# Kernel tuning notes

Hardware: AMD Instinct MI355X
Metric: run time of the kernel (lower is better)

Reference implementation:

```python
import jax, jax.numpy as jnp
import numpy as np

N_NODES = 50000
N_EDGES = 800000
D_IN, HIDDEN, OUT, K = 96, 64, 16, 3


def _glorot(key, shape):
    fan_in, fan_out = shape[-2], shape[-1]
    lim = (6.0 / (fan_in + fan_out)) ** 0.5
    return jax.random.uniform(key, shape, jnp.float32, -lim, lim)


def setup_inputs() -> dict:
    key = jax.random.key(0)
    k1, k2, k3, k4 = jax.random.split(key, 4)
    x = jax.random.normal(k1, (N_NODES, D_IN), dtype=jnp.float32)
    edge_index = jax.random.randint(k2, (2, N_EDGES), 0, N_NODES, dtype=jnp.int64)
    # ChebConv params: K stacked linear maps per layer + one bias per layer
    W1 = _glorot(k3, (K, D_IN, HIDDEN))
    b1 = jnp.zeros((HIDDEN,), jnp.float32)
    W2 = _glorot(k4, (K, HIDDEN, OUT))
    b2 = jnp.zeros((OUT,), jnp.float32)
    return {"x": x, "edge_index": edge_index, "W1": W1, "b1": b1, "W2": W2, "b2": b2}


def _cheb_norm(edge_index, num_nodes):
    # PyG ChebConv norm with normalization='sym', lambda_max=2.0:
    # Ltilde = (2/lmax)*(I - D^-1/2 A D^-1/2) - I = -D^-1/2 A D^-1/2 (diag weight 0)
    src, dst = edge_index[0], edge_index[1]
    ones = jnp.ones((edge_index.shape[1],), jnp.float32)
    deg = jax.ops.segment_sum(ones, src, num_segments=num_nodes)
    dis = jnp.where(deg > 0, jax.lax.rsqrt(jnp.maximum(deg, 1.0)), 0.0)
    return -dis[src] * dis[dst]  # [E]


def _cheb_conv(x, src, dst, w, W, b, num_nodes):
    # Chebyshev recurrence: Tx0=x, Tx1=L x, Txk=2 L Tx_{k-1} - Tx_{k-2}
    def prop(h):  # sparse matvec: scatter-add of weighted source features
        return jax.ops.segment_sum(w[:, None] * h[src], dst, num_segments=num_nodes)

    Tx0 = x
    out = Tx0 @ W[0]
    Tx1 = prop(Tx0)
    out = out + Tx1 @ W[1]
    for k in range(2, W.shape[0]):
        Tx2 = 2.0 * prop(Tx1) - Tx0
        out = out + Tx2 @ W[k]
        Tx0, Tx1 = Tx1, Tx2
    return out + b


def reference(x, edge_index, W1, b1, W2, b2):
    num_nodes = x.shape[0]
    src, dst = edge_index[0], edge_index[1]
    w = _cheb_norm(edge_index, num_nodes)
    h = jax.nn.relu(_cheb_conv(x, src, dst, w, W1, b1, num_nodes))
    return _cheb_conv(h, src, dst, w, W2, b2, num_nodes)
```

## Files before the change

kernel.cpp:

```cpp
#include <hip/hip_runtime.h>

#define N_NODES 50000
#define N_EDGES 800000
#define D_IN 96
#define HID 64
#define D_OUT 16

#define EPB 2048
#define NBLK_E ((N_EDGES + EPB - 1) / EPB)
#define BSHIFT 7
#define NBKT ((N_NODES + 127) / 128)
#define DCAP 2560
#define PACK_TOT (3 * D_IN * HID + 3 * HID * D_OUT)
#define PACK_BLKS (PACK_TOT / 256)

typedef unsigned short u16;
typedef unsigned int u32;
typedef __attribute__((ext_vector_type(4))) float f32x4;
typedef __attribute__((ext_vector_type(8))) short bf16x8;

__device__ inline float bflo(u32 v) { union { u32 i; float f; } u; u.i = v << 16; return u.f; }
__device__ inline float bfhi(u32 v) { union { u32 i; float f; } u; u.i = v & 0xffff0000u; return u.f; }
__device__ inline u16 f2bf(float f) {
    union { float f; u32 i; } u; u.f = f;
    return (u16)((u.i + 0x7fffu + ((u.i >> 16) & 1u)) >> 16);
}
__device__ inline u32 pack2(float lo, float hi) {
    return (u32)f2bf(lo) | ((u32)f2bf(hi) << 16);
}


__global__ __launch_bounds__(256)
void passA(const int* __restrict__ src, const int* __restrict__ dst,
           int* __restrict__ blk_cnt_src, int* __restrict__ blk_cnt_dst,
           const float* __restrict__ W1, const float* __restrict__ W2,
           u16* __restrict__ Pb1, u16* __restrict__ Pb2) {
    const int t = threadIdx.x, blk = blockIdx.x;
    if (blk >= NBLK_E) {
        int tt = (blk - NBLK_E) * 256 + t;
        if (tt < 3 * D_IN * HID) {
            int j = tt & 7, rest = tt >> 3;
            int c = rest % 192, i = (rest / 192) * 8 + j;
            int kc = c / 64, o = c % 64;
            Pb1[tt] = f2bf(W1[((long)kc * D_IN + i) * HID + o]);
        } else if (tt < PACK_TOT) {
            int t2 = tt - 3 * D_IN * HID;
            int j = t2 & 7, rest = t2 >> 3;
            int c = rest % 48, i = (rest / 48) * 8 + j;
            int kc = c / 16, o = c % 16;
            Pb2[t2] = f2bf(W2[((long)kc * HID + i) * D_OUT + o]);
        }
        return;
    }
    __shared__ int hs[NBKT], hd[NBKT];
    for (int i = t; i < NBKT; i += 256) { hs[i] = 0; hd[i] = 0; }
    __syncthreads();
    const int e0 = blk * EPB;
    const int e1 = (e0 + EPB < N_EDGES) ? e0 + EPB : N_EDGES;
    for (int e = e0 + t; e < e1; e += 256) {
        atomicAdd(&hs[src[e] >> BSHIFT], 1);
        atomicAdd(&hd[dst[e] >> BSHIFT], 1);
    }
    __syncthreads();
    for (int b = t; b < NBKT; b += 256) {
        blk_cnt_src[b * NBLK_E + blk] = hs[b];
        blk_cnt_dst[b * NBLK_E + blk] = hd[b];
    }
}

__global__ __launch_bounds__(64)
void passB(int* __restrict__ blk_cnt_src, int* __restrict__ blk_cnt_dst,
           int* __restrict__ tot_src, int* __restrict__ tot_dst) {
    const int b = blockIdx.x;
    int* cnt; int* tot;
    if (b < NBKT) { cnt = blk_cnt_dst + b * NBLK_E;          tot = tot_dst + b; }
    else          { cnt = blk_cnt_src + (b - NBKT) * NBLK_E; tot = tot_src + (b - NBKT); }
    const int lane = threadIdx.x;
    int carry = 0;
    for (int base0 = 0; base0 < NBLK_E; base0 += 64) {
        int i = base0 + lane;
        int v = (i < NBLK_E) ? cnt[i] : 0;
        int incl = v;
        #pragma unroll
        for (int off = 1; off < 64; off <<= 1) {
            int x = __shfl_up(incl, off);
            if (lane >= off) incl += x;
        }
        if (i < NBLK_E) cnt[i] = carry + incl - v;
        carry += __shfl(incl, 63);
    }
    if (lane == 0) *tot = carry;
}

__global__ __launch_bounds__(256)
void passB2(const int* __restrict__ tot_src, const int* __restrict__ tot_dst,
            int* __restrict__ base_src, int* __restrict__ base_dst, int* __restrict__ row_ptr) {
    __shared__ int s[512];
    const int t = threadIdx.x;
    for (int pass = 0; pass < 2; ++pass) {
        const int* tot = pass ? tot_src : tot_dst;
        int* bas = pass ? base_src : base_dst;
        s[t]       = (t < NBKT) ? tot[t] : 0;
        s[t + 256] = (t + 256 < NBKT) ? tot[t + 256] : 0;
        __syncthreads();
        for (int off = 1; off < 512; off <<= 1) {
            int a1 = (t >= off) ? s[t - off] : 0;
            int a2 = (t + 256 >= off) ? s[t + 256 - off] : 0;
            __syncthreads();
            s[t] += a1; s[t + 256] += a2;
            __syncthreads();
        }
        if (t == 0) bas[0] = 0;
        if (t < NBKT) bas[t + 1] = s[t];
        if (t + 256 < NBKT) bas[t + 257] = s[t + 256];
        __syncthreads();
    }
    if (t == 0) row_ptr[N_NODES] = N_EDGES;
}

__global__ __launch_bounds__(256)
void passC(const int* __restrict__ src, const int* __restrict__ dst,
           const int* __restrict__ blk_off_src, const int* __restrict__ blk_off_dst,
           const int* __restrict__ base_src, const int* __restrict__ base_dst,
           u16* __restrict__ sorted_srconly, u32* __restrict__ sorted_pair) {
    __shared__ int cs[NBKT], cd[NBKT];
    const int t = threadIdx.x, blk = blockIdx.x;
    for (int b = t; b < NBKT; b += 256) {
        cs[b] = base_src[b] + blk_off_src[b * NBLK_E + blk];
        cd[b] = base_dst[b] + blk_off_dst[b * NBLK_E + blk];
    }
    __syncthreads();
    const int e0 = blk * EPB;
    const int e1 = (e0 + EPB < N_EDGES) ? e0 + EPB : N_EDGES;
    for (int e = e0 + t; e < e1; e += 256) {
        int sv = src[e], dv = dst[e];
        int ps = atomicAdd(&cs[sv >> BSHIFT], 1);
        sorted_srconly[ps] = (u16)sv;
        int pd = atomicAdd(&cd[dv >> BSHIFT], 1);
        sorted_pair[pd] = ((u32)dv << 16) | (u32)sv;
    }
}

__global__ __launch_bounds__(256)
void passD(const int* __restrict__ base_src, const u16* __restrict__ sorted_srconly,
           const int* __restrict__ base_dst, const u32* __restrict__ sorted_pair,
           float* __restrict__ dis, int* __restrict__ row_ptr, u16* __restrict__ wsrc) {
    const int t = threadIdx.x;
    if (blockIdx.x < NBKT) {
        __shared__ int hist[128];
        const int b = blockIdx.x;
        if (t < 128) hist[t] = 0;
        __syncthreads();
        const int eb = base_src[b], ee = base_src[b + 1];
        for (int i = eb + t; i < ee; i += 256)
            atomicAdd(&hist[sorted_srconly[i] & 127], 1);
        __syncthreads();
        const int node = (b << BSHIFT) + t;
        if (t < 128 && node < N_NODES) {
            int c = hist[t];
            dis[node] = c > 0 ? rsqrtf((float)c) : 0.0f;
        }
        return;
    }
    __shared__ u32 s_p[DCAP];
    __shared__ int hist[128];
    __shared__ int cur[128];
    const int b = blockIdx.x - NBKT;
    if (t < 128) hist[t] = 0;
    __syncthreads();
    const int eb = base_dst[b], ee = base_dst[b + 1];
    const int cnt = ee - eb;
    const int stage = cnt < DCAP ? cnt : DCAP;
    for (int i = t; i < stage; i += 256) {
        u32 v = sorted_pair[eb + i];
        s_p[i] = v;
        atomicAdd(&hist[(v >> 16) & 127], 1);
    }
    for (int i = stage + t; i < cnt; i += 256)
        atomicAdd(&hist[(sorted_pair[eb + i] >> 16) & 127], 1);
    __syncthreads();
    if (t < 64) {
        int v0 = hist[2 * t], v1 = hist[2 * t + 1];
        int p = v0 + v1;
        int incl = p;
        #pragma unroll
        for (int off = 1; off < 64; off <<= 1) {
            int x = __shfl_up(incl, off);
            if (t >= off) incl += x;
        }
        int excl = incl - p;
        cur[2 * t] = excl;
        cur[2 * t + 1] = excl + v0;
        int node = (b << BSHIFT) + 2 * t;
        if (node < N_NODES) row_ptr[node] = eb + excl;
        if (node + 1 < N_NODES) row_ptr[node + 1] = eb + excl + v0;
    }
    __syncthreads();
    for (int i = t; i < stage; i += 256) {
        u32 v = s_p[i];
        int slot = atomicAdd(&cur[(v >> 16) & 127], 1);
        wsrc[eb + slot] = (u16)(v & 0xFFFF);
    }
    for (int i = stage + t; i < cnt; i += 256) {
        u32 v = sorted_pair[eb + i];
        int slot = atomicAdd(&cur[(v >> 16) & 127], 1);
        wsrc[eb + slot] = (u16)(v & 0xFFFF);
    }
}


template<int K, int NC, int LDZ, int CPK, long CBS, bool AF32>
__global__ __launch_bounds__(256)
void gemm_mfma(const void* __restrict__ Av, const u16* __restrict__ P, u16* __restrict__ Z,
               const float* __restrict__ dis, u16* __restrict__ Zs) {
    constexpr int KT = K / 32;
    constexpr int TOT = K * NC;
    __shared__ u16 sP[TOT];
    for (int idx = threadIdx.x * 8; idx < TOT; idx += 2048)
        *(uint4*)&sP[idx] = *(const uint4*)&P[idx];
    __syncthreads();
    const int lane = threadIdx.x & 63;
    const int tile = blockIdx.x * 4 + (threadIdx.x >> 6);
    if (tile * 16 >= N_NODES) return;
    const int node0 = tile * 16;
    const int sub = lane >> 4, r16 = lane & 15;
    float dis4[4];
    #pragma unroll
    for (int r = 0; r < 4; ++r) dis4[r] = dis[node0 + sub * 4 + r];
    bf16x8 a[KT];
    if (AF32) {
        const float* ar = (const float*)Av + (long)(node0 + r16) * K + sub * 8;
        #pragma unroll
        for (int kt = 0; kt < KT; ++kt) {
            float4 a0 = *(const float4*)(ar + kt * 32);
            float4 a1 = *(const float4*)(ar + kt * 32 + 4);
            union { bf16x8 v; uint4 q; } u;
            u.q.x = pack2(a0.x, a0.y); u.q.y = pack2(a0.z, a0.w);
            u.q.z = pack2(a1.x, a1.y); u.q.w = pack2(a1.z, a1.w);
            a[kt] = u.v;
        }
    } else {
        const u16* ar = (const u16*)Av + (long)(node0 + r16) * K + sub * 8;
        #pragma unroll
        for (int kt = 0; kt < KT; ++kt)
            a[kt] = *(const bf16x8*)(ar + kt * 32);
    }
    #pragma unroll
    for (int ct = 0; ct < NC / 16; ++ct) {
        f32x4 acc = {0.f, 0.f, 0.f, 0.f};
        #pragma unroll
        for (int kt = 0; kt < KT; ++kt) {
            bf16x8 bfr = *(const bf16x8*)&sP[((kt * 4 + sub) * NC + ct * 16 + r16) * 8];
            acc = __builtin_amdgcn_mfma_f32_16x16x32_bf16(a[kt], bfr, acc, 0, 0, 0);
        }
        const long rowoff = (long)(node0 + sub * 4) * LDZ + (ct % CPK) * 16 + r16;
        u16* zp = Z + (long)(ct / CPK) * CBS + rowoff;
        #pragma unroll
        for (int r = 0; r < 4; ++r)
            zp[(long)r * LDZ] = f2bf(acc[r]);
        if (ct / CPK == 2) {
            u16* zs = Zs + rowoff;
            #pragma unroll
            for (int r = 0; r < 4; ++r)
                zs[(long)r * LDZ] = f2bf(acc[r] * dis4[r]);
        }
    }
}


#define EPI_S 0
#define EPI_H 1
#define EPI_OUT 2

__device__ inline void sum8(float (&acc)[8], uint4 q) {
    acc[0] += bflo(q.x); acc[1] += bfhi(q.x);
    acc[2] += bflo(q.y); acc[3] += bfhi(q.y);
    acc[4] += bflo(q.z); acc[5] += bfhi(q.z);
    acc[6] += bflo(q.w); acc[7] += bfhi(q.w);
}

template<int F, int NPB, int CAP, int EPI>
__global__ __launch_bounds__(256)
void gather_prop(const int* __restrict__ row_ptr, const u16* __restrict__ ws,
                 const u16* __restrict__ g,
                 const u16* __restrict__ aux1,
                 const u16* __restrict__ aux2,
                 const float* __restrict__ bias,
                 const float* __restrict__ dis,
                 void* __restrict__ outp) {
    __shared__ u16 s_p[CAP];
    __shared__ int s_beg[NPB + 1];
    const int tid = threadIdx.x;
    const int node0 = blockIdx.x * NPB;
    if (tid <= NPB) {
        int n = node0 + tid;
        s_beg[tid] = row_ptr[n > N_NODES ? N_NODES : n];
    }
    __syncthreads();
    const int ebeg = s_beg[0];
    const int cnt = s_beg[NPB] - ebeg;
    const int stage = cnt < CAP ? cnt : CAP;
    for (int e = tid; e < stage; e += 256)
        s_p[e] = ws[ebeg + e];
    __syncthreads();
    constexpr int CPN = F / 8;
    const int nl = tid / CPN;
    const int node = node0 + nl;
    if (nl >= NPB || node >= N_NODES) return;
    const int c8 = (tid % CPN) * 8;
    float acc[8];
    #pragma unroll
    for (int j = 0; j < 8; ++j) acc[j] = 0.0f;
    const int beg = s_beg[nl] - ebeg;
    const int end = s_beg[nl + 1] - ebeg;
    const int mid = end < stage ? end : stage;
    int e = beg;
    for (; e + 8 <= mid; e += 8) {
        int p0 = s_p[e],     p1 = s_p[e + 1], p2 = s_p[e + 2], p3 = s_p[e + 3];
        int p4 = s_p[e + 4], p5 = s_p[e + 5], p6 = s_p[e + 6], p7 = s_p[e + 7];
        uint4 q0 = *(const uint4*)(g + (long)p0 * F + c8);
        uint4 q1 = *(const uint4*)(g + (long)p1 * F + c8);
        uint4 q2 = *(const uint4*)(g + (long)p2 * F + c8);
        uint4 q3 = *(const uint4*)(g + (long)p3 * F + c8);
        uint4 q4 = *(const uint4*)(g + (long)p4 * F + c8);
        uint4 q5 = *(const uint4*)(g + (long)p5 * F + c8);
        uint4 q6 = *(const uint4*)(g + (long)p6 * F + c8);
        uint4 q7 = *(const uint4*)(g + (long)p7 * F + c8);
        sum8(acc, q0); sum8(acc, q1); sum8(acc, q2); sum8(acc, q3);
        sum8(acc, q4); sum8(acc, q5); sum8(acc, q6); sum8(acc, q7);
    }
    for (; e + 4 <= mid; e += 4) {
        int p0 = s_p[e], p1 = s_p[e + 1], p2 = s_p[e + 2], p3 = s_p[e + 3];
        uint4 q0 = *(const uint4*)(g + (long)p0 * F + c8);
        uint4 q1 = *(const uint4*)(g + (long)p1 * F + c8);
        uint4 q2 = *(const uint4*)(g + (long)p2 * F + c8);
        uint4 q3 = *(const uint4*)(g + (long)p3 * F + c8);
        sum8(acc, q0); sum8(acc, q1); sum8(acc, q2); sum8(acc, q3);
    }
    for (; e < mid; ++e)
        sum8(acc, *(const uint4*)(g + (long)s_p[e] * F + c8));
    for (e = (beg > stage ? beg : stage); e < end; ++e)
        sum8(acc, *(const uint4*)(g + (long)ws[ebeg + e] * F + c8));
    const float dd = dis[node];
    if (EPI == EPI_S) {
        const float m1 = dd, m2 = -2.0f * dd * dd;
        const uint4 z1 = *(const uint4*)(aux1 + (long)node * F + c8);
        uint4 r;
        r.x = pack2(fmaf(m1, bflo(z1.x), m2 * acc[0]), fmaf(m1, bfhi(z1.x), m2 * acc[1]));
        r.y = pack2(fmaf(m1, bflo(z1.y), m2 * acc[2]), fmaf(m1, bfhi(z1.y), m2 * acc[3]));
        r.z = pack2(fmaf(m1, bflo(z1.z), m2 * acc[4]), fmaf(m1, bfhi(z1.z), m2 * acc[5]));
        r.w = pack2(fmaf(m1, bflo(z1.w), m2 * acc[6]), fmaf(m1, bfhi(z1.w), m2 * acc[7]));
        *(uint4*)((u16*)outp + (long)node * F + c8) = r;
    } else {
        const uint4 z0 = *(const uint4*)(aux1 + (long)node * F + c8);
        const uint4 z2 = *(const uint4*)(aux2 + (long)node * F + c8);
        const float* bb = bias + c8;
        float v0 = bflo(z0.x) - bflo(z2.x) - dd * acc[0] + bb[0];
        float v1 = bfhi(z0.x) - bfhi(z2.x) - dd * acc[1] + bb[1];
        float v2 = bflo(z0.y) - bflo(z2.y) - dd * acc[2] + bb[2];
        float v3 = bfhi(z0.y) - bfhi(z2.y) - dd * acc[3] + bb[3];
        float v4 = bflo(z0.z) - bflo(z2.z) - dd * acc[4] + bb[4];
        float v5 = bfhi(z0.z) - bfhi(z2.z) - dd * acc[5] + bb[5];
        float v6 = bflo(z0.w) - bflo(z2.w) - dd * acc[6] + bb[6];
        float v7 = bfhi(z0.w) - bfhi(z2.w) - dd * acc[7] + bb[7];
        if (EPI == EPI_H) {
            uint4 r;
            r.x = pack2(fmaxf(v0, 0.f), fmaxf(v1, 0.f));
            r.y = pack2(fmaxf(v2, 0.f), fmaxf(v3, 0.f));
            r.z = pack2(fmaxf(v4, 0.f), fmaxf(v5, 0.f));
            r.w = pack2(fmaxf(v6, 0.f), fmaxf(v7, 0.f));
            *(uint4*)((u16*)outp + (long)node * F + c8) = r;
        } else {
            float* op = (float*)outp + (long)node * F + c8;
            *(float4*)op = make_float4(v0, v1, v2, v3);
            *(float4*)(op + 4) = make_float4(v4, v5, v6, v7);
        }
    }
}


extern "C" void kernel_launch(void* const* d_in, const int* in_sizes, int n_in,
                              void* d_out, int out_size, void* d_ws, size_t ws_size,
                              hipStream_t stream) {
    const float* x  = (const float*)d_in[0];
    const int*   ei = (const int*)d_in[1];
    const float* W1 = (const float*)d_in[2];
    const float* b1 = (const float*)d_in[3];
    const float* W2 = (const float*)d_in[4];
    const float* b2 = (const float*)d_in[5];
    const int* src = ei;
    const int* dst = ei + N_EDGES;

    float* dis          = (float*)d_ws;
    int*   row_ptr      = (int*)(dis + N_NODES);
    int*   blk_cnt_src  = row_ptr + 50016;
    int*   blk_cnt_dst  = blk_cnt_src + 152896;
    int*   tot_src      = blk_cnt_dst + 152896;
    int*   tot_dst      = tot_src + 512;
    int*   base_src     = tot_dst + 512;
    int*   base_dst     = base_src + 512;
    u16*   srconly      = (u16*)(base_dst + 512);
    u32*   sorted_pair  = (u32*)(srconly + N_EDGES);
    u16*   wsrc         = (u16*)(sorted_pair + N_EDGES);
    u16*   Z            = wsrc + N_EDGES;
    u16*   Zs           = Z  + (long)3 * N_NODES * HID;
    u16*   S            = Zs + (long)N_NODES * HID;
    u16*   hb           = S  + (long)N_NODES * HID;
    u16*   Zp           = hb + (long)N_NODES * HID;
    u16*   Zsp          = Zp + (long)3 * N_NODES * D_OUT;
    u16*   Sp           = Zsp + (long)N_NODES * D_OUT;
    u16*   Pb1          = Sp + (long)N_NODES * D_OUT;
    u16*   Pb2          = Pb1 + 18432;

    const long PZ  = (long)N_NODES * HID;
    const long PZp = (long)N_NODES * D_OUT;

    passA<<<NBLK_E + PACK_BLKS, 256, 0, stream>>>(src, dst, blk_cnt_src, blk_cnt_dst,
                                                  W1, W2, Pb1, Pb2);
    passB<<<2 * NBKT, 64, 0, stream>>>(blk_cnt_src, blk_cnt_dst, tot_src, tot_dst);
    passB2<<<1, 256, 0, stream>>>(tot_src, tot_dst, base_src, base_dst, row_ptr);
    passC<<<NBLK_E, 256, 0, stream>>>(src, dst, blk_cnt_src, blk_cnt_dst, base_src, base_dst,
                                      srconly, sorted_pair);
    passD<<<2 * NBKT, 256, 0, stream>>>(base_src, srconly, base_dst, sorted_pair,
                                        dis, row_ptr, wsrc);

    const int GB = (N_NODES / 16 + 3) / 4;
    gemm_mfma<D_IN, 192, HID, 4, (long)N_NODES * HID, true><<<GB, 256, 0, stream>>>(
        x, Pb1, Z, dis, Zs);
    gather_prop<HID, 32, 1024, EPI_S><<<(N_NODES + 31) / 32, 256, 0, stream>>>(
        row_ptr, wsrc, Zs, Z + PZ, nullptr, nullptr, dis, S);
    gather_prop<HID, 32, 1024, EPI_H><<<(N_NODES + 31) / 32, 256, 0, stream>>>(
        row_ptr, wsrc, S, Z, Z + 2 * PZ, b1, dis, hb);

    gemm_mfma<HID, 48, D_OUT, 1, (long)N_NODES * D_OUT, false><<<GB, 256, 0, stream>>>(
        hb, Pb2, Zp, dis, Zsp);
    gather_prop<D_OUT, 128, 3072, EPI_S><<<(N_NODES + 127) / 128, 256, 0, stream>>>(
        row_ptr, wsrc, Zsp, Zp + PZp, nullptr, nullptr, dis, Sp);
    gather_prop<D_OUT, 128, 3072, EPI_OUT><<<(N_NODES + 127) / 128, 256, 0, stream>>>(
        row_ptr, wsrc, Sp, Zp, Zp + 2 * PZp, b2, dis, (float*)d_out);
}
```

Before: 122.8 us.

## Fold bucket prefix scan into passC/passD and precombine Z0-Z2 in GEMM

Removes the single-block passB2 launch: each passC block redoes the 512-entry bucket scan itself, and each passD block computes its base offset by summing earlier bucket totals. The GEMM epilogue now writes Z0-Z2 as one combined array instead of separate Z0 and Z2 planes, so the final gather epilogues read one fewer auxiliary array. This cuts one kernel launch and some memory traffic, at the cost of redundant scan work in every passC and passD block.

```diff
diff --git a/kernel.cpp b/kernel.cpp
--- a/kernel.cpp
+++ b/kernel.cpp
@@ -93,13 +93,17 @@
 }
 
 __global__ __launch_bounds__(256)
-void passB2(const int* __restrict__ tot_src, const int* __restrict__ tot_dst,
-            int* __restrict__ base_src, int* __restrict__ base_dst, int* __restrict__ row_ptr) {
+void passC(const int* __restrict__ src, const int* __restrict__ dst,
+           const int* __restrict__ blk_off_src, const int* __restrict__ blk_off_dst,
+           const int* __restrict__ tot_src, const int* __restrict__ tot_dst,
+           u16* __restrict__ sorted_srconly, u32* __restrict__ sorted_pair) {
     __shared__ int s[512];
-    const int t = threadIdx.x;
+    __shared__ int cs[NBKT], cd[NBKT];
+    const int t = threadIdx.x, blk = blockIdx.x;
     for (int pass = 0; pass < 2; ++pass) {
         const int* tot = pass ? tot_src : tot_dst;
-        int* bas = pass ? base_src : base_dst;
+        const int* bo  = pass ? blk_off_src : blk_off_dst;
+        int* cx = pass ? cs : cd;
         s[t]       = (t < NBKT) ? tot[t] : 0;
         s[t + 256] = (t + 256 < NBKT) ? tot[t + 256] : 0;
         __syncthreads();
@@ -110,26 +114,10 @@
             s[t] += a1; s[t + 256] += a2;
             __syncthreads();
         }
-        if (t == 0) bas[0] = 0;
-        if (t < NBKT) bas[t + 1] = s[t];
-        if (t + 256 < NBKT) bas[t + 257] = s[t + 256];
+        if (t < NBKT) cx[t] = s[t] - tot[t] + bo[t * NBLK_E + blk];
+        if (t + 256 < NBKT) cx[t + 256] = s[t + 256] - tot[t + 256] + bo[(t + 256) * NBLK_E + blk];
         __syncthreads();
     }
-    if (t == 0) row_ptr[N_NODES] = N_EDGES;
-}
-
-__global__ __launch_bounds__(256)
-void passC(const int* __restrict__ src, const int* __restrict__ dst,
-           const int* __restrict__ blk_off_src, const int* __restrict__ blk_off_dst,
-           const int* __restrict__ base_src, const int* __restrict__ base_dst,
-           u16* __restrict__ sorted_srconly, u32* __restrict__ sorted_pair) {
-    __shared__ int cs[NBKT], cd[NBKT];
-    const int t = threadIdx.x, blk = blockIdx.x;
-    for (int b = t; b < NBKT; b += 256) {
-        cs[b] = base_src[b] + blk_off_src[b * NBLK_E + blk];
-        cd[b] = base_dst[b] + blk_off_dst[b * NBLK_E + blk];
-    }
-    __syncthreads();
     const int e0 = blk * EPB;
     const int e1 = (e0 + EPB < N_EDGES) ? e0 + EPB : N_EDGES;
     for (int e = e0 + t; e < e1; e += 256) {
@@ -142,16 +130,30 @@
 }
 
 __global__ __launch_bounds__(256)
-void passD(const int* __restrict__ base_src, const u16* __restrict__ sorted_srconly,
-           const int* __restrict__ base_dst, const u32* __restrict__ sorted_pair,
+void passD(const int* __restrict__ tot_src, const u16* __restrict__ sorted_srconly,
+           const int* __restrict__ tot_dst, const u32* __restrict__ sorted_pair,
            float* __restrict__ dis, int* __restrict__ row_ptr, u16* __restrict__ wsrc) {
+    __shared__ int sred[256];
+    __shared__ int hist[128];
+    __shared__ int cur[128];
+    __shared__ u32 s_p[DCAP];
     const int t = threadIdx.x;
-    if (blockIdx.x < NBKT) {
-        __shared__ int hist[128];
-        const int b = blockIdx.x;
-        if (t < 128) hist[t] = 0;
+    const bool isSrc = blockIdx.x < NBKT;
+    const int b = isSrc ? blockIdx.x : blockIdx.x - NBKT;
+    const int* tot = isSrc ? tot_src : tot_dst;
+    int part = 0;
+    for (int i = t; i < b; i += 256) part += tot[i];
+    sred[t] = part;
+    if (t < 128) hist[t] = 0;
+    __syncthreads();
+    #pragma unroll
+    for (int off = 128; off > 0; off >>= 1) {
+        if (t < off) sred[t] += sred[t + off];
         __syncthreads();
-        const int eb = base_src[b], ee = base_src[b + 1];
+    }
+    const int eb = sred[0];
+    const int ee = eb + tot[b];
+    if (isSrc) {
         for (int i = eb + t; i < ee; i += 256)
             atomicAdd(&hist[sorted_srconly[i] & 127], 1);
         __syncthreads();
@@ -162,13 +164,7 @@
         }
         return;
     }
-    __shared__ u32 s_p[DCAP];
-    __shared__ int hist[128];
-    __shared__ int cur[128];
-    const int b = blockIdx.x - NBKT;
-    if (t < 128) hist[t] = 0;
-    __syncthreads();
-    const int eb = base_dst[b], ee = base_dst[b + 1];
+    if (b == 0 && t == 0) row_ptr[N_NODES] = N_EDGES;
     const int cnt = ee - eb;
     const int stage = cnt < DCAP ? cnt : DCAP;
     for (int i = t; i < stage; i += 256) {
@@ -209,10 +205,11 @@
 }
 
 
-template<int K, int NC, int LDZ, int CPK, long CBS, bool AF32>
+template<int K, int NC, int LDZ, int CPK, bool AF32>
 __global__ __launch_bounds__(256)
-void gemm_mfma(const void* __restrict__ Av, const u16* __restrict__ P, u16* __restrict__ Z,
-               const float* __restrict__ dis, u16* __restrict__ Zs) {
+void gemm_mfma(const void* __restrict__ Av, const u16* __restrict__ P,
+               u16* __restrict__ D02, u16* __restrict__ Z1, u16* __restrict__ Zs,
+               const float* __restrict__ dis) {
     constexpr int KT = K / 32;
     constexpr int TOT = K * NC;
     __shared__ u16 sP[TOT];
@@ -245,25 +242,33 @@
         for (int kt = 0; kt < KT; ++kt)
             a[kt] = *(const bf16x8*)(ar + kt * 32);
     }
-    #pragma unroll
-    for (int ct = 0; ct < NC / 16; ++ct) {
+    auto cc = [&](int ct) {
         f32x4 acc = {0.f, 0.f, 0.f, 0.f};
         #pragma unroll
         for (int kt = 0; kt < KT; ++kt) {
             bf16x8 bfr = *(const bf16x8*)&sP[((kt * 4 + sub) * NC + ct * 16 + r16) * 8];
             acc = __builtin_amdgcn_mfma_f32_16x16x32_bf16(a[kt], bfr, acc, 0, 0, 0);
         }
-        const long rowoff = (long)(node0 + sub * 4) * LDZ + (ct % CPK) * 16 + r16;
-        u16* zp = Z + (long)(ct / CPK) * CBS + rowoff;
+        return acc;
+    };
+    #pragma unroll
+    for (int i = 0; i < CPK; ++i) {
+        f32x4 acc0 = cc(i);
+        f32x4 acc2 = cc(2 * CPK + i);
+        const long rowoff = (long)(node0 + sub * 4) * LDZ + i * 16 + r16;
+        #pragma unroll
+        for (int r = 0; r < 4; ++r) {
+            D02[rowoff + (long)r * LDZ] = f2bf(acc0[r] - acc2[r]);
+            Zs[rowoff + (long)r * LDZ]  = f2bf(acc2[r] * dis4[r]);
+        }
+    }
+    #pragma unroll
+    for (int i = 0; i < CPK; ++i) {
+        f32x4 acc1 = cc(CPK + i);
+        const long rowoff = (long)(node0 + sub * 4) * LDZ + i * 16 + r16;
         #pragma unroll
         for (int r = 0; r < 4; ++r)
-            zp[(long)r * LDZ] = f2bf(acc[r]);
-        if (ct / CPK == 2) {
-            u16* zs = Zs + rowoff;
-            #pragma unroll
-            for (int r = 0; r < 4; ++r)
-                zs[(long)r * LDZ] = f2bf(acc[r] * dis4[r]);
-        }
+            Z1[rowoff + (long)r * LDZ] = f2bf(acc1[r]);
     }
 }
 
@@ -284,7 +289,6 @@
 void gather_prop(const int* __restrict__ row_ptr, const u16* __restrict__ ws,
                  const u16* __restrict__ g,
                  const u16* __restrict__ aux1,
-                 const u16* __restrict__ aux2,
                  const float* __restrict__ bias,
                  const float* __restrict__ dis,
                  void* __restrict__ outp) {
@@ -353,16 +357,15 @@
         *(uint4*)((u16*)outp + (long)node * F + c8) = r;
     } else {
         const uint4 z0 = *(const uint4*)(aux1 + (long)node * F + c8);
-        const uint4 z2 = *(const uint4*)(aux2 + (long)node * F + c8);
         const float* bb = bias + c8;
-        float v0 = bflo(z0.x) - bflo(z2.x) - dd * acc[0] + bb[0];
-        float v1 = bfhi(z0.x) - bfhi(z2.x) - dd * acc[1] + bb[1];
-        float v2 = bflo(z0.y) - bflo(z2.y) - dd * acc[2] + bb[2];
-        float v3 = bfhi(z0.y) - bfhi(z2.y) - dd * acc[3] + bb[3];
-        float v4 = bflo(z0.z) - bflo(z2.z) - dd * acc[4] + bb[4];
-        float v5 = bfhi(z0.z) - bfhi(z2.z) - dd * acc[5] + bb[5];
-        float v6 = bflo(z0.w) - bflo(z2.w) - dd * acc[6] + bb[6];
-        float v7 = bfhi(z0.w) - bfhi(z2.w) - dd * acc[7] + bb[7];
+        float v0 = bflo(z0.x) - dd * acc[0] + bb[0];
+        float v1 = bfhi(z0.x) - dd * acc[1] + bb[1];
+        float v2 = bflo(z0.y) - dd * acc[2] + bb[2];
+        float v3 = bfhi(z0.y) - dd * acc[3] + bb[3];
+        float v4 = bflo(z0.z) - dd * acc[4] + bb[4];
+        float v5 = bfhi(z0.z) - dd * acc[5] + bb[5];
+        float v6 = bflo(z0.w) - dd * acc[6] + bb[6];
+        float v7 = bfhi(z0.w) - dd * acc[7] + bb[7];
         if (EPI == EPI_H) {
             uint4 r;
             r.x = pack2(fmaxf(v0, 0.f), fmaxf(v1, 0.f));
@@ -397,45 +400,39 @@
     int*   blk_cnt_dst  = blk_cnt_src + 152896;
     int*   tot_src      = blk_cnt_dst + 152896;
     int*   tot_dst      = tot_src + 512;
-    int*   base_src     = tot_dst + 512;
-    int*   base_dst     = base_src + 512;
-    u16*   srconly      = (u16*)(base_dst + 512);
+    u16*   srconly      = (u16*)(tot_dst + 512);
     u32*   sorted_pair  = (u32*)(srconly + N_EDGES);
     u16*   wsrc         = (u16*)(sorted_pair + N_EDGES);
-    u16*   Z            = wsrc + N_EDGES;
-    u16*   Zs           = Z  + (long)3 * N_NODES * HID;
-    u16*   S            = Zs + (long)N_NODES * HID;
-    u16*   hb           = S  + (long)N_NODES * HID;
-    u16*   Zp           = hb + (long)N_NODES * HID;
-    u16*   Zsp          = Zp + (long)3 * N_NODES * D_OUT;
-    u16*   Sp           = Zsp + (long)N_NODES * D_OUT;
-    u16*   Pb1          = Sp + (long)N_NODES * D_OUT;
+    u16*   D02          = wsrc + N_EDGES;
+    u16*   Z1b          = D02 + (long)N_NODES * HID;
+    u16*   Zs           = Z1b + (long)N_NODES * HID;
+    u16*   S            = Zs  + (long)N_NODES * HID;
+    u16*   hb           = S   + (long)N_NODES * HID;
+    u16*   D02p         = hb  + (long)N_NODES * HID;
+    u16*   Z1p          = D02p + (long)N_NODES * D_OUT;
+    u16*   Zsp          = Z1p  + (long)N_NODES * D_OUT;
+    u16*   Sp           = Zsp  + (long)N_NODES * D_OUT;
+    u16*   Pb1          = Sp   + (long)N_NODES * D_OUT;
     u16*   Pb2          = Pb1 + 18432;
-
-    const long PZ  = (long)N_NODES * HID;
-    const long PZp = (long)N_NODES * D_OUT;
 
     passA<<<NBLK_E + PACK_BLKS, 256, 0, stream>>>(src, dst, blk_cnt_src, blk_cnt_dst,
                                                   W1, W2, Pb1, Pb2);
     passB<<<2 * NBKT, 64, 0, stream>>>(blk_cnt_src, blk_cnt_dst, tot_src, tot_dst);
-    passB2<<<1, 256, 0, stream>>>(tot_src, tot_dst, base_src, base_dst, row_ptr);
-    passC<<<NBLK_E, 256, 0, stream>>>(src, dst, blk_cnt_src, blk_cnt_dst, base_src, base_dst,
+    passC<<<NBLK_E, 256, 0, stream>>>(src, dst, blk_cnt_src, blk_cnt_dst, tot_src, tot_dst,
                                       srconly, sorted_pair);
-    passD<<<2 * NBKT, 256, 0, stream>>>(base_src, srconly, base_dst, sorted_pair,
+    passD<<<2 * NBKT, 256, 0, stream>>>(tot_src, srconly, tot_dst, sorted_pair,
                                         dis, row_ptr, wsrc);
 
     const int GB = (N_NODES / 16 + 3) / 4;
-    gemm_mfma<D_IN, 192, HID, 4, (long)N_NODES * HID, true><<<GB, 256, 0, stream>>>(
-        x, Pb1, Z, dis, Zs);
+    gemm_mfma<D_IN, 192, HID, 4, true><<<GB, 256, 0, stream>>>(x, Pb1, D02, Z1b, Zs, dis);
     gather_prop<HID, 32, 1024, EPI_S><<<(N_NODES + 31) / 32, 256, 0, stream>>>(
-        row_ptr, wsrc, Zs, Z + PZ, nullptr, nullptr, dis, S);
+        row_ptr, wsrc, Zs, Z1b, nullptr, dis, S);
     gather_prop<HID, 32, 1024, EPI_H><<<(N_NODES + 31) / 32, 256, 0, stream>>>(
-        row_ptr, wsrc, S, Z, Z + 2 * PZ, b1, dis, hb);
-
-    gemm_mfma<HID, 48, D_OUT, 1, (long)N_NODES * D_OUT, false><<<GB, 256, 0, stream>>>(
-        hb, Pb2, Zp, dis, Zsp);
+        row_ptr, wsrc, S, D02, b1, dis, hb);
+
+    gemm_mfma<HID, 48, D_OUT, 1, false><<<GB, 256, 0, stream>>>(hb, Pb2, D02p, Z1p, Zsp, dis);
     gather_prop<D_OUT, 128, 3072, EPI_S><<<(N_NODES + 127) / 128, 256, 0, stream>>>(
-        row_ptr, wsrc, Zsp, Zp + PZp, nullptr, nullptr, dis, Sp);
+        row_ptr, wsrc, Zsp, Z1p, nullptr, dis, Sp);
     gather_prop<D_OUT, 128, 3072, EPI_OUT><<<(N_NODES + 127) / 128, 256, 0, stream>>>(
-        row_ptr, wsrc, Sp, Zp, Zp + 2 * PZp, b2, dis, (float*)d_out);
-}
+        row_ptr, wsrc, Sp, D02p, b2, dis, (float*)d_out);
+}
```

Result: no change. 120.9 us (-1.5%).
